# Performance work log

Measured on AMD Instinct MI355X. Metric: run time of the kernel, lower is better.

## Reference

```python
import jax, jax.numpy as jnp
import numpy as np

B, C, H, W = 32, 512, 32, 32  # in_dims = token_dim = 512, num_heads = 1
D = 512  # token_dim * num_heads
EPS = 1e-12  # torch F.normalize eps


def l2norm(x, axis):
    n = jnp.sqrt(jnp.sum(x * x, axis=axis, keepdims=True))
    return x / jnp.maximum(n, EPS)


def setup_inputs() -> dict:
    key = jax.random.key(0)
    ks = jax.random.split(key, 10)
    s = 1.0 / np.sqrt(D)
    return {
        "x_4d": jax.random.normal(ks[0], (B, C, H, W), dtype=jnp.float32),
        "Wq": jax.random.uniform(ks[1], (D, D), jnp.float32, -s, s),
        "bq": jax.random.uniform(ks[2], (D,), jnp.float32, -s, s),
        "Wk": jax.random.uniform(ks[3], (D, D), jnp.float32, -s, s),
        "bk": jax.random.uniform(ks[4], (D,), jnp.float32, -s, s),
        "w_g": jax.random.normal(ks[5], (D, 1), dtype=jnp.float32),
        "Wp": jax.random.uniform(ks[6], (D, D), jnp.float32, -s, s),
        "bp": jax.random.uniform(ks[7], (D,), jnp.float32, -s, s),
        "Wf": jax.random.uniform(ks[8], (D, D), jnp.float32, -s, s),
        "bf": jax.random.uniform(ks[9], (D,), jnp.float32, -s, s),
    }


def reference(x_4d, Wq, bq, Wk, bk, w_g, Wp, bp, Wf, bf):
    b, c, h, w = x_4d.shape
    n = h * w
    scale = D ** (-0.5)
    x = x_4d.reshape(b, c, n).transpose(0, 2, 1)  # [b, n, c]
    query = l2norm(jnp.einsum("bnc,dc->bnd", x, Wq) + bq, axis=-1)  # [b, n, d]
    key = l2norm(jnp.einsum("bnc,dc->bnd", x, Wk) + bk, axis=-1)    # [b, n, d]
    query_weight = query @ w_g                      # [b, n, 1]
    a = l2norm(query_weight * scale, axis=1)        # normalize over sequence dim
    g = jnp.sum(a * query, axis=1)                  # [b, d] global context
    out = jnp.einsum("bnd,ed->bne", g[:, None, :] * key, Wp) + bp + query
    out = jnp.einsum("bnd,ed->bne", out, Wf) + bf
    return out.transpose(0, 2, 1).reshape(b, c, h, w)
```

## Files before the change

kernel.cpp:

```cpp
#include <hip/hip_runtime.h>
#include <hip/hip_bf16.h>
#include <math.h>

#define B_ 32
#define D_ 512
#define N_ 1024
#define T_ 32768
#define SCALE 0.04419417382415922f

typedef unsigned short u16;
typedef __attribute__((ext_vector_type(8))) short bf16x8;
typedef __attribute__((ext_vector_type(4))) float f32x4;
typedef __attribute__((ext_vector_type(8))) unsigned short u16x8;
typedef __attribute__((ext_vector_type(4))) unsigned int u32x4;

__device__ __forceinline__ u16 bf16_rn(float f) {
    unsigned u = __float_as_uint(f);
    u += 0x7FFFu + ((u >> 16) & 1u);
    return (u16)(u >> 16);
}
__device__ __forceinline__ float bf16f(u16 h) {
    return __uint_as_float(((unsigned)h) << 16);
}
__device__ __forceinline__ unsigned pkbf(float a, float b) {
    __hip_bfloat162 h = __float22bfloat162_rn(make_float2(a, b));
    return *reinterpret_cast<unsigned*>(&h);
}

__device__ __forceinline__ void g2l16(const u16* g, u16* lds) {
    __builtin_amdgcn_global_load_lds(
        (const __attribute__((address_space(1))) unsigned int*)g,
        (__attribute__((address_space(3))) unsigned int*)lds, 16, 0, 0);
}

__device__ __forceinline__ float waveRedSum(float v) {
#pragma unroll
    for (int off = 32; off > 0; off >>= 1) v += __shfl_xor(v, off, 64);
    return v;
}


__global__ __launch_bounds__(256) void convw_k(const float* __restrict__ W0,
                                               const float* __restrict__ W1,
                                               const float* __restrict__ W2,
                                               u16* O0, u16* O1, u16* O2) {
    const int s = blockIdx.y;
    const float* src = (s == 0) ? W0 : ((s == 1) ? W1 : W2);
    u16* O = (s == 0) ? O0 : ((s == 1) ? O1 : O2);
    const size_t i0 = (size_t)blockIdx.x * 2048 + threadIdx.x * 8;
    u16 o[8];
#pragma unroll
    for (int j = 0; j < 8; ++j) o[j] = bf16_rn(src[i0 + j]);
    *(u16x8*)&O[i0] = *(const u16x8*)&o[0];
}


__global__ __launch_bounds__(256) void finalize_k(float* __restrict__ ssqQ,
                                                  float* __restrict__ ssqK,
                                                  float* __restrict__ qwr,
                                                  float* __restrict__ Sb) {
    __shared__ float red[4];
    const int i = blockIdx.x * 256 + threadIdx.x;
    const float rq = 1.f / fmaxf(sqrtf(ssqQ[i]), 1e-12f);
    ssqQ[i] = rq;
    const float rk = 1.f / fmaxf(sqrtf(ssqK[i]), 1e-12f);
    ssqK[i] = rk;
    const float qwp = qwr[i] * rq;
    qwr[i] = qwp * rq;
    float s = qwp * qwp;
    s = waveRedSum(s);
    if ((threadIdx.x & 63) == 0) red[threadIdx.x >> 6] = s;
    __syncthreads();
    if (threadIdx.x == 0)
        atomicAdd(Sb + (blockIdx.x >> 2), red[0] + red[1] + red[2] + red[3]);
}

__global__ __launch_bounds__(512) void gctx_k(const float* __restrict__ qw,
                                              const u16* __restrict__ Qn,
                                              float* __restrict__ g) {
    const int b = blockIdx.y;
    const int n0 = blockIdx.x * 128;
    const int d = threadIdx.x;
    const u16* qp = Qn + ((size_t)b * N_ + n0) * D_ + d;
    const float* wp = qw + (size_t)b * N_ + n0;
    float acc = 0.f;
    for (int n = 0; n < 128; ++n) acc += wp[n] * bf16f(qp[(size_t)n * D_]);
    atomicAdd(g + b * D_ + d, acc);
}

__global__ __launch_bounds__(256) void scalewp_k(const float* __restrict__ Wp,
                                                 const float* __restrict__ g,
                                                 const float* __restrict__ Sb,
                                                 u16* __restrict__ WpG) {
    const int b = blockIdx.y;
    const float fb = SCALE / fmaxf(SCALE * sqrtf(Sb[b]), 1e-12f);
    const size_t f0 = (size_t)blockIdx.x * 2048 + threadIdx.x * 8;
    const int c = (int)(f0 & 511);
    u16 o[8];
#pragma unroll
    for (int j = 0; j < 8; ++j)
        o[j] = bf16_rn(Wp[f0 + j] * g[b * D_ + c + j] * fb);
    *(u16x8*)&WpG[(size_t)b * 262144 + f0] = *(const u16x8*)&o[0];
}

__global__ __launch_bounds__(512, 4) void mgemm0(
        const float* __restrict__ x, const u16* __restrict__ B0,
        const u16* __restrict__ B1,
        const float* __restrict__ bias0, const float* __restrict__ bias1,
        const float* __restrict__ wg,
        float* __restrict__ ssqQ, float* __restrict__ ssqK,
        float* __restrict__ qwr, u16* uout0, u16* uout1) {
    __shared__ u16 As[128 * 64];
    __shared__ u16 Bs[256 * 64];
    const int tid = threadIdx.x;
    const int l = tid & 63, w = tid >> 6;
    const int gid = blockIdx.x;
    const int xcd = gid & 7;
    const int bx = (gid >> 3) & 3;
    const int by = (gid >> 5) * 8 + xcd;
    const int t0 = by * 128;
    const bool sel = bx >= 2;
    const int e0 = (bx & 1) * 256;
    const u16* B = sel ? B1 : B0;
    const float* bias = sel ? bias1 : bias0;
    u16* uout = sel ? uout1 : uout0;
    float* ssq = sel ? ssqK : ssqQ;
    const int batch0 = t0 >> 10;

    const float* xbase = x + (((size_t)(batch0 * D_ + w * 8)) << 10) +
                         (t0 & 1023) + 2 * l;
    const int r0 = 2 * l, r1 = 2 * l + 1;
    u16* wA0 = &As[r0 * 64 + ((w ^ (r0 & 7)) * 8)];
    u16* wA1 = &As[r1 * 64 + ((w ^ (r1 & 7)) * 8)];
    size_t gB[4];
    u16* ldsB[4];
#pragma unroll
    for (int i = 0; i < 4; ++i) {
        const int rr = w * 32 + i * 8 + (l >> 3);
        gB[i] = (size_t)(e0 + rr) * 512 + (((l & 7) ^ (rr & 7)) * 8);
        ldsB[i] = Bs + (w * 32 + i * 8) * 64;
    }

    const int wr = w >> 2, wc = w & 3, kg = l >> 4, r16 = l & 15;
    int aoff[4][2], boff[4][2];
#pragma unroll
    for (int f = 0; f < 4; ++f)
#pragma unroll
        for (int h = 0; h < 2; ++h) {
            const int ra = wr * 64 + f * 16 + r16;
            aoff[f][h] = ra * 64 + (((h * 4 + kg) ^ (ra & 7)) * 8);
            const int rb = wc * 64 + f * 16 + r16;
            boff[f][h] = rb * 64 + (((h * 4 + kg) ^ (rb & 7)) * 8);
        }

    f32x4 acc[4][4];
#pragma unroll
    for (int i = 0; i < 4; ++i)
#pragma unroll
        for (int j = 0; j < 4; ++j) acc[i][j] = 0.f;

    float2 va[8];
#pragma unroll
    for (int j = 0; j < 8; ++j)
        va[j] = *(const float2*)(xbase + ((size_t)j << 10));

#pragma unroll 1
    for (int s = 0; s < 8; ++s) {
        const int c0 = s * 64;
        __syncthreads();
        {
            u32x4 p0, p1;
#pragma unroll
            for (int jj = 0; jj < 4; ++jj) {
                p0[jj] = pkbf(va[2 * jj].x, va[2 * jj + 1].x);
                p1[jj] = pkbf(va[2 * jj].y, va[2 * jj + 1].y);
            }
            *(u32x4*)wA0 = p0;
            *(u32x4*)wA1 = p1;
        }
#pragma unroll
        for (int i = 0; i < 4; ++i) g2l16(B + gB[i] + c0, ldsB[i]);
        __syncthreads();
        if (s < 7) {
#pragma unroll
            for (int j = 0; j < 8; ++j)
                va[j] = *(const float2*)(xbase + ((size_t)(c0 + 64 + j) << 10));
        }
#pragma unroll
        for (int h = 0; h < 2; ++h) {
            bf16x8 av[4], bv[4];
#pragma unroll
            for (int f = 0; f < 4; ++f) {
                av[f] = *(const bf16x8*)&As[aoff[f][h]];
                bv[f] = *(const bf16x8*)&Bs[boff[f][h]];
            }
#pragma unroll
            for (int i = 0; i < 4; ++i)
#pragma unroll
                for (int j = 0; j < 4; ++j)
                    acc[i][j] = __builtin_amdgcn_mfma_f32_16x16x32_bf16(
                        av[i], bv[j], acc[i][j], 0, 0, 0);
        }
    }

    const int mb = wr * 64 + kg * 4;
    const int nb = wc * 64 + r16;
    float bb[4], wgv[4];
#pragma unroll
    for (int fn = 0; fn < 4; ++fn) {
        const int n = e0 + nb + fn * 16;
        bb[fn] = bias[n];
        wgv[fn] = sel ? 0.f : wg[n];
    }
#pragma unroll
    for (int fm = 0; fm < 4; ++fm) {
#pragma unroll
        for (int q = 0; q < 4; ++q) {
            const int m = t0 + mb + fm * 16 + q;
            float s2 = 0.f, wd = 0.f;
#pragma unroll
            for (int fn = 0; fn < 4; ++fn) {
                const float val = acc[fm][fn][q] + bb[fn];
                uout[(size_t)m * 512 + e0 + nb + fn * 16] = bf16_rn(val);
                s2 += val * val;
                wd += val * wgv[fn];
            }
#pragma unroll
            for (int off = 1; off < 16; off <<= 1) {
                s2 += __shfl_xor(s2, off, 64);
                wd += __shfl_xor(wd, off, 64);
            }
            if (r16 == 0) {
                atomicAdd(ssq + m, s2);
                if (!sel) atomicAdd(qwr + m, wd);
            }
        }
    }
}

template <int MODE>
__global__ __launch_bounds__(256) void mgemm12(
        const u16* __restrict__ A, const u16* __restrict__ B0,
        const float* __restrict__ bias,
        const float* __restrict__ rsA, const float* __restrict__ rsQ,
        u16* uout, float* __restrict__ fout) {
    __shared__ u16 As[128 * 64];
    __shared__ u16 Bs[128 * 64];
    const int tid = threadIdx.x;
    const int l = tid & 63, w = tid >> 6;
    const int gid = blockIdx.x;
    const int xcd = gid & 7;

    int rowt, col, batch;
    if (MODE == 1) {
        const int j = gid >> 3;
        batch = (j >> 5) * 8 + xcd;
        const int r = j & 31;
        rowt = batch * 8 + (r >> 2);
        col = r & 3;
    } else {
        col = (gid >> 3) & 3;
        rowt = (gid >> 5) * 8 + xcd;
        batch = rowt >> 3;
    }
    const int tt0 = rowt * 128;
    const int e0 = col * 128;
    const u16* B = (MODE == 1) ? B0 + (size_t)batch * 262144 : B0;
    const int arow0 = (MODE == 2) ? e0 : tt0;
    const int brow0 = (MODE == 2) ? tt0 : e0;

    size_t gA[4], gB[4];
    u16 *ldsA[4], *ldsB[4];
#pragma unroll
    for (int i = 0; i < 4; ++i) {
        const int rr = w * 32 + i * 8 + (l >> 3);
        const int sw = ((l & 7) ^ (rr & 7)) * 8;
        gA[i] = (size_t)(arow0 + rr) * 512 + sw;
        gB[i] = (size_t)(brow0 + rr) * 512 + sw;
        ldsA[i] = As + (w * 32 + i * 8) * 64;
        ldsB[i] = Bs + (w * 32 + i * 8) * 64;
    }

    const int wr = w >> 1, wc = w & 1, kg = l >> 4, r16 = l & 15;
    int aoff[4][2], boff[4][2];
#pragma unroll
    for (int f = 0; f < 4; ++f)
#pragma unroll
        for (int h = 0; h < 2; ++h) {
            const int ra = wr * 64 + f * 16 + r16;
            aoff[f][h] = ra * 64 + (((h * 4 + kg) ^ (ra & 7)) * 8);
            const int rb = wc * 64 + f * 16 + r16;
            boff[f][h] = rb * 64 + (((h * 4 + kg) ^ (rb & 7)) * 8);
        }

    f32x4 acc[4][4];
#pragma unroll
    for (int i = 0; i < 4; ++i)
#pragma unroll
        for (int j = 0; j < 4; ++j) acc[i][j] = 0.f;

#pragma unroll 1
    for (int c0 = 0; c0 < 512; c0 += 64) {
        __syncthreads();
#pragma unroll
        for (int i = 0; i < 4; ++i) {
            g2l16(A + gA[i] + c0, ldsA[i]);
            g2l16(B + gB[i] + c0, ldsB[i]);
        }
        __syncthreads();
#pragma unroll
        for (int h = 0; h < 2; ++h) {
            bf16x8 av[4], bv[4];
#pragma unroll
            for (int f = 0; f < 4; ++f) {
                av[f] = *(const bf16x8*)&As[aoff[f][h]];
                bv[f] = *(const bf16x8*)&Bs[boff[f][h]];
            }
#pragma unroll
            for (int i = 0; i < 4; ++i)
#pragma unroll
                for (int j = 0; j < 4; ++j)
                    acc[i][j] = __builtin_amdgcn_mfma_f32_16x16x32_bf16(
                        av[i], bv[j], acc[i][j], 0, 0, 0);
        }
    }

    const int mb = wr * 64 + kg * 4;
    const int nb = wc * 64 + r16;
    if (MODE == 1) {
#pragma unroll
        for (int fm = 0; fm < 4; ++fm) {
            const int m0 = tt0 + mb + fm * 16;
            const float4 ra4 = *(const float4*)(rsA + m0);
            const float4 rq4 = *(const float4*)(rsQ + m0);
            const float ra_[4] = {ra4.x, ra4.y, ra4.z, ra4.w};
            const float rq_[4] = {rq4.x, rq4.y, rq4.z, rq4.w};
#pragma unroll
            for (int fn = 0; fn < 4; ++fn) {
                const int n = e0 + nb + fn * 16;
                const float bb = bias[n];
#pragma unroll
                for (int q = 0; q < 4; ++q) {
                    const size_t idx = (size_t)(m0 + q) * 512 + n;
                    const float val = acc[fm][fn][q] * ra_[q] + bb +
                                      bf16f(uout[idx]) * rq_[q];
                    uout[idx] = bf16_rn(val);
                }
            }
        }
    } else {
#pragma unroll
        for (int fm = 0; fm < 4; ++fm)
#pragma unroll
            for (int fn = 0; fn < 4; ++fn) {
                const int ntok = (tt0 & 1023) + nb + fn * 16;
#pragma unroll
                for (int q = 0; q < 4; ++q) {
                    const int e = e0 + mb + fm * 16 + q;
                    fout[((size_t)(batch * D_ + e) << 10) + ntok] =
                        acc[fm][fn][q] + bias[e];
                }
            }
    }
}


extern "C" void kernel_launch(void* const* d_in, const int* in_sizes, int n_in,
                              void* d_out, int out_size, void* d_ws, size_t ws_size,
                              hipStream_t stream) {
    const float* x  = (const float*)d_in[0];
    const float* Wq = (const float*)d_in[1];
    const float* bq = (const float*)d_in[2];
    const float* Wk = (const float*)d_in[3];
    const float* bk = (const float*)d_in[4];
    const float* wg = (const float*)d_in[5];
    const float* Wp = (const float*)d_in[6];
    const float* bp = (const float*)d_in[7];
    const float* Wf = (const float*)d_in[8];
    const float* bf = (const float*)d_in[9];
    float* out = (float*)d_out;

    char* Wb = (char*)d_ws;
    u16* WpG = (u16*)Wb;
    u16* Qn  = (u16*)(Wb + 33554432ull);
    u16* Kn  = (u16*)(Wb + 67108864ull);
    char* S  = Wb + 100663296ull;
    u16* Wqbf = (u16*)S;
    u16* Wkbf = (u16*)(S + 524288ull);
    u16* Wfbf = (u16*)(S + 1048576ull);
    char* Z   = S + 1572864ull;
    float* SSQQ = (float*)Z;
    float* SSQK = (float*)(Z + 131072ull);
    float* QWR  = (float*)(Z + 262144ull);
    float* G    = (float*)(Z + 393216ull);
    float* Sb   = (float*)(Z + 458752ull);
    const size_t ZBYTES = 458752ull + 128ull;

    const dim3 blk(256);

    convw_k<<<dim3(128, 3), blk, 0, stream>>>(Wq, Wk, Wf, Wqbf, Wkbf, Wfbf);
    hipMemsetAsync(Z, 0, ZBYTES, stream);
    mgemm0<<<dim3(1024), dim3(512), 0, stream>>>(x, Wqbf, Wkbf, bq, bk, wg,
                                                 SSQQ, SSQK, QWR, Qn, Kn);
    finalize_k<<<dim3(128), blk, 0, stream>>>(SSQQ, SSQK, QWR, Sb);
    gctx_k<<<dim3(8, B_), dim3(512), 0, stream>>>(QWR, Qn, G);
    scalewp_k<<<dim3(128, B_), blk, 0, stream>>>(Wp, G, Sb, WpG);
    mgemm12<1><<<dim3(1024), blk, 0, stream>>>(Kn, WpG, bp, SSQK, SSQQ, Qn,
                                               nullptr);
    mgemm12<2><<<dim3(1024), blk, 0, stream>>>(Wfbf, Qn, bf, nullptr, nullptr,
                                               nullptr, out);
}
```

Measured before the change: 148.2 us.

## Double-buffer B tile in LDS and prefetch next K-step in mgemm0

Adds a second LDS buffer for the weight tile so the next K-slice's global-to-LDS copy is issued before the MFMA work on the current slice. Explicit vmcnt waits and raw s_barriers replace the two __syncthreads per iteration, and the K loop is fully unrolled. The A-tile swizzle is changed to key on row pairs, which is meant to cut LDS bank conflicts. LDS use grows by 32KB per block, which may lower occupancy, and the hand-counted vmcnt value must match the number of outstanding loads to stay correct.

Measured after the change: 194.5 us. 1.31x slower.

```diff
diff --git a/kernel.cpp b/kernel.cpp
--- a/kernel.cpp
+++ b/kernel.cpp
@@ -111,7 +111,7 @@
         float* __restrict__ ssqQ, float* __restrict__ ssqK,
         float* __restrict__ qwr, u16* uout0, u16* uout1) {
     __shared__ u16 As[128 * 64];
-    __shared__ u16 Bs[256 * 64];
+    __shared__ u16 Bs[2][256 * 64];
     const int tid = threadIdx.x;
     const int l = tid & 63, w = tid >> 6;
     const int gid = blockIdx.x;
@@ -130,15 +130,16 @@
     const float* xbase = x + (((size_t)(batch0 * D_ + w * 8)) << 10) +
                          (t0 & 1023) + 2 * l;
     const int r0 = 2 * l, r1 = 2 * l + 1;
-    u16* wA0 = &As[r0 * 64 + ((w ^ (r0 & 7)) * 8)];
-    u16* wA1 = &As[r1 * 64 + ((w ^ (r1 & 7)) * 8)];
+    const int sA = w ^ (l & 7);
+    u16* wA0 = &As[r0 * 64 + sA * 8];
+    u16* wA1 = &As[r1 * 64 + sA * 8];
     size_t gB[4];
-    u16* ldsB[4];
+    int lB[4];
 #pragma unroll
     for (int i = 0; i < 4; ++i) {
         const int rr = w * 32 + i * 8 + (l >> 3);
         gB[i] = (size_t)(e0 + rr) * 512 + (((l & 7) ^ (rr & 7)) * 8);
-        ldsB[i] = Bs + (w * 32 + i * 8) * 64;
+        lB[i] = (w * 32 + i * 8) * 64;
     }
 
     const int wr = w >> 2, wc = w & 3, kg = l >> 4, r16 = l & 15;
@@ -148,7 +149,7 @@
 #pragma unroll
         for (int h = 0; h < 2; ++h) {
             const int ra = wr * 64 + f * 16 + r16;
-            aoff[f][h] = ra * 64 + (((h * 4 + kg) ^ (ra & 7)) * 8);
+            aoff[f][h] = ra * 64 + (((h * 4 + kg) ^ ((ra >> 1) & 7)) * 8);
             const int rb = wc * 64 + f * 16 + r16;
             boff[f][h] = rb * 64 + (((h * 4 + kg) ^ (rb & 7)) * 8);
         }
@@ -163,11 +164,11 @@
 #pragma unroll
     for (int j = 0; j < 8; ++j)
         va[j] = *(const float2*)(xbase + ((size_t)j << 10));
-
-#pragma unroll 1
+#pragma unroll
+    for (int i = 0; i < 4; ++i) g2l16(B + gB[i], &Bs[0][lB[i]]);
+
+#pragma unroll
     for (int s = 0; s < 8; ++s) {
-        const int c0 = s * 64;
-        __syncthreads();
         {
             u32x4 p0, p1;
 #pragma unroll
@@ -178,21 +179,31 @@
             *(u32x4*)wA0 = p0;
             *(u32x4*)wA1 = p1;
         }
-#pragma unroll
-        for (int i = 0; i < 4; ++i) g2l16(B + gB[i] + c0, ldsB[i]);
-        __syncthreads();
         if (s < 7) {
 #pragma unroll
             for (int j = 0; j < 8; ++j)
-                va[j] = *(const float2*)(xbase + ((size_t)(c0 + 64 + j) << 10));
-        }
+                va[j] = *(const float2*)(xbase +
+                                         ((size_t)((s + 1) * 64 + j) << 10));
+#pragma unroll
+            for (int i = 0; i < 4; ++i)
+                g2l16(B + gB[i] + (s + 1) * 64, &Bs[(s + 1) & 1][lB[i]]);
+        }
+        __builtin_amdgcn_sched_barrier(0);
+        if (s < 7) {
+            asm volatile("s_waitcnt vmcnt(12)" ::: "memory");
+        } else {
+            asm volatile("s_waitcnt vmcnt(0)" ::: "memory");
+        }
+        asm volatile("s_waitcnt lgkmcnt(0)" ::: "memory");
+        __builtin_amdgcn_sched_barrier(0);
+        __builtin_amdgcn_s_barrier();
 #pragma unroll
         for (int h = 0; h < 2; ++h) {
             bf16x8 av[4], bv[4];
 #pragma unroll
             for (int f = 0; f < 4; ++f) {
                 av[f] = *(const bf16x8*)&As[aoff[f][h]];
-                bv[f] = *(const bf16x8*)&Bs[boff[f][h]];
+                bv[f] = *(const bf16x8*)&Bs[s & 1][boff[f][h]];
             }
 #pragma unroll
             for (int i = 0; i < 4; ++i)
@@ -201,6 +212,7 @@
                     acc[i][j] = __builtin_amdgcn_mfma_f32_16x16x32_bf16(
                         av[i], bv[j], acc[i][j], 0, 0, 0);
         }
+        if (s < 7) __builtin_amdgcn_s_barrier();
     }
 
     const int mb = wr * 64 + kg * 4;
```

## Fold finalize kernel into consumers and fix LDS swizzle for A tile

Applied to the files above, without the earlier changes.

Removes the separate finalize kernel by recomputing the reciprocal norms and the per-batch sequence-norm sum inside gctx_k, scalewp_k and the mgemm12 epilogue, saving one launch and a read-modify-write pass. It also changes the A-tile LDS XOR swizzle in mgemm0 to key on row pairs, matching the two-row writes, to cut bank conflicts. The wd shuffle reduction now runs only for the Q half. In exchange, every scalewp block redoes a 1024-element reduction and the epilogues add redundant sqrt/div work.

Measured after the change: 154.2 us. 4.1% more time.

```diff
diff --git a/kernel.cpp b/kernel.cpp
--- a/kernel.cpp
+++ b/kernel.cpp
@@ -37,6 +37,9 @@
 #pragma unroll
     for (int off = 32; off > 0; off >>= 1) v += __shfl_xor(v, off, 64);
     return v;
+}
+__device__ __forceinline__ float rnorm_s(float ssq) {
+    return 1.f / fmaxf(sqrtf(ssq), 1e-12f);
 }
 
 
@@ -55,45 +58,45 @@
 }
 
 
-__global__ __launch_bounds__(256) void finalize_k(float* __restrict__ ssqQ,
-                                                  float* __restrict__ ssqK,
-                                                  float* __restrict__ qwr,
-                                                  float* __restrict__ Sb) {
+__global__ __launch_bounds__(512) void gctx_k(const float* __restrict__ ssqQ,
+                                              const float* __restrict__ qwr,
+                                              const u16* __restrict__ Qn,
+                                              float* __restrict__ g) {
+    __shared__ float coeff[128];
+    const int b = blockIdx.y;
+    const int n0 = blockIdx.x * 128;
+    const int d = threadIdx.x;
+    if (d < 128) {
+        const int r = b * N_ + n0 + d;
+        const float rq = rnorm_s(ssqQ[r]);
+        coeff[d] = qwr[r] * rq * rq;
+    }
+    __syncthreads();
+    const u16* qp = Qn + ((size_t)b * N_ + n0) * D_ + d;
+    float acc = 0.f;
+    for (int n = 0; n < 128; ++n) acc += coeff[n] * bf16f(qp[(size_t)n * D_]);
+    atomicAdd(g + b * D_ + d, acc);
+}
+
+__global__ __launch_bounds__(256) void scalewp_k(const float* __restrict__ Wp,
+                                                 const float* __restrict__ g,
+                                                 const float* __restrict__ ssqQ,
+                                                 const float* __restrict__ qwr,
+                                                 u16* __restrict__ WpG) {
     __shared__ float red[4];
-    const int i = blockIdx.x * 256 + threadIdx.x;
-    const float rq = 1.f / fmaxf(sqrtf(ssqQ[i]), 1e-12f);
-    ssqQ[i] = rq;
-    const float rk = 1.f / fmaxf(sqrtf(ssqK[i]), 1e-12f);
-    ssqK[i] = rk;
-    const float qwp = qwr[i] * rq;
-    qwr[i] = qwp * rq;
-    float s = qwp * qwp;
+    const int b = blockIdx.y;
+    float s = 0.f;
+#pragma unroll
+    for (int j = 0; j < 4; ++j) {
+        const int r = b * N_ + threadIdx.x * 4 + j;
+        const float t = qwr[r] * rnorm_s(ssqQ[r]);
+        s += t * t;
+    }
     s = waveRedSum(s);
     if ((threadIdx.x & 63) == 0) red[threadIdx.x >> 6] = s;
     __syncthreads();
-    if (threadIdx.x == 0)
-        atomicAdd(Sb + (blockIdx.x >> 2), red[0] + red[1] + red[2] + red[3]);
-}
-
-__global__ __launch_bounds__(512) void gctx_k(const float* __restrict__ qw,
-                                              const u16* __restrict__ Qn,
-                                              float* __restrict__ g) {
-    const int b = blockIdx.y;
-    const int n0 = blockIdx.x * 128;
-    const int d = threadIdx.x;
-    const u16* qp = Qn + ((size_t)b * N_ + n0) * D_ + d;
-    const float* wp = qw + (size_t)b * N_ + n0;
-    float acc = 0.f;
-    for (int n = 0; n < 128; ++n) acc += wp[n] * bf16f(qp[(size_t)n * D_]);
-    atomicAdd(g + b * D_ + d, acc);
-}
-
-__global__ __launch_bounds__(256) void scalewp_k(const float* __restrict__ Wp,
-                                                 const float* __restrict__ g,
-                                                 const float* __restrict__ Sb,
-                                                 u16* __restrict__ WpG) {
-    const int b = blockIdx.y;
-    const float fb = SCALE / fmaxf(SCALE * sqrtf(Sb[b]), 1e-12f);
+    const float S = red[0] + red[1] + red[2] + red[3];
+    const float fb = SCALE / fmaxf(SCALE * sqrtf(S), 1e-12f);
     const size_t f0 = (size_t)blockIdx.x * 2048 + threadIdx.x * 8;
     const int c = (int)(f0 & 511);
     u16 o[8];
@@ -130,8 +133,9 @@
     const float* xbase = x + (((size_t)(batch0 * D_ + w * 8)) << 10) +
                          (t0 & 1023) + 2 * l;
     const int r0 = 2 * l, r1 = 2 * l + 1;
-    u16* wA0 = &As[r0 * 64 + ((w ^ (r0 & 7)) * 8)];
-    u16* wA1 = &As[r1 * 64 + ((w ^ (r1 & 7)) * 8)];
+    const int sA = w ^ (l & 7);
+    u16* wA0 = &As[r0 * 64 + sA * 8];
+    u16* wA1 = &As[r1 * 64 + sA * 8];
     size_t gB[4];
     u16* ldsB[4];
 #pragma unroll
@@ -148,7 +152,7 @@
 #pragma unroll
         for (int h = 0; h < 2; ++h) {
             const int ra = wr * 64 + f * 16 + r16;
-            aoff[f][h] = ra * 64 + (((h * 4 + kg) ^ (ra & 7)) * 8);
+            aoff[f][h] = ra * 64 + (((h * 4 + kg) ^ ((ra >> 1) & 7)) * 8);
             const int rb = wc * 64 + f * 16 + r16;
             boff[f][h] = rb * 64 + (((h * 4 + kg) ^ (rb & 7)) * 8);
         }
@@ -226,9 +230,12 @@
                 wd += val * wgv[fn];
             }
 #pragma unroll
-            for (int off = 1; off < 16; off <<= 1) {
+            for (int off = 1; off < 16; off <<= 1)
                 s2 += __shfl_xor(s2, off, 64);
-                wd += __shfl_xor(wd, off, 64);
+            if (!sel) {
+#pragma unroll
+                for (int off = 1; off < 16; off <<= 1)
+                    wd += __shfl_xor(wd, off, 64);
             }
             if (r16 == 0) {
                 atomicAdd(ssq + m, s2);
@@ -333,8 +340,10 @@
             const int m0 = tt0 + mb + fm * 16;
             const float4 ra4 = *(const float4*)(rsA + m0);
             const float4 rq4 = *(const float4*)(rsQ + m0);
-            const float ra_[4] = {ra4.x, ra4.y, ra4.z, ra4.w};
-            const float rq_[4] = {rq4.x, rq4.y, rq4.z, rq4.w};
+            const float ra_[4] = {rnorm_s(ra4.x), rnorm_s(ra4.y),
+                                  rnorm_s(ra4.z), rnorm_s(ra4.w)};
+            const float rq_[4] = {rnorm_s(rq4.x), rnorm_s(rq4.y),
+                                  rnorm_s(rq4.z), rnorm_s(rq4.w)};
 #pragma unroll
             for (int fn = 0; fn < 4; ++fn) {
                 const int n = e0 + nb + fn * 16;
@@ -393,8 +402,7 @@
     float* SSQK = (float*)(Z + 131072ull);
     float* QWR  = (float*)(Z + 262144ull);
     float* G    = (float*)(Z + 393216ull);
-    float* Sb   = (float*)(Z + 458752ull);
-    const size_t ZBYTES = 458752ull + 128ull;
+    const size_t ZBYTES = 458752ull;
 
     const dim3 blk(256);
 
@@ -402,9 +410,8 @@
     hipMemsetAsync(Z, 0, ZBYTES, stream);
     mgemm0<<<dim3(1024), dim3(512), 0, stream>>>(x, Wqbf, Wkbf, bq, bk, wg,
                                                  SSQQ, SSQK, QWR, Qn, Kn);
-    finalize_k<<<dim3(128), blk, 0, stream>>>(SSQQ, SSQK, QWR, Sb);
-    gctx_k<<<dim3(8, B_), dim3(512), 0, stream>>>(QWR, Qn, G);
-    scalewp_k<<<dim3(128, B_), blk, 0, stream>>>(Wp, G, Sb, WpG);
+    gctx_k<<<dim3(8, B_), dim3(512), 0, stream>>>(SSQQ, QWR, Qn, G);
+    scalewp_k<<<dim3(128, B_), blk, 0, stream>>>(Wp, G, SSQQ, QWR, WpG);
     mgemm12<1><<<dim3(1024), blk, 0, stream>>>(Kn, WpG, bp, SSQK, SSQQ, Qn,
                                                nullptr);
     mgemm12<2><<<dim3(1024), blk, 0, stream>>>(Wfbf, Qn, bf, nullptr, nullptr,
```
